# Performance work log

Hardware: AMD Instinct MI355X
Metric: run time of the kernel (lower is better)

## Reference

```python
import jax, jax.numpy as jnp
import numpy as np

# Module config (matches init_kwargs)
SHAPE = (32, 32)          # wire grid
KERNEL = (3, 3)           # window per dim
NUM_LAYERS = 4
NINPUTS = int(np.prod(KERNEL))        # 9
NPOS = 2 ** NINPUTS                   # 512 possible boolean input combos


def _bitmask():
    # itertools.product(range(2), repeat=NINPUTS) then transpose -> (NINPUTS, NPOS)
    # combination j, window-element m has bit (j >> (NINPUTS-1-m)) & 1
    j = jnp.arange(NPOS)
    m = jnp.arange(NINPUTS)
    return ((j[None, :] >> (NINPUTS - 1 - m)[:, None]) & 1).astype(jnp.float32)


def _convolve(x):
    # x: (B, H, W) -> (B, H, W, K) wrapped sliding windows (im2col via rolls),
    # faithful to ASIC.convolve with kernel_offset='center'.
    out = x
    for d, k in enumerate(KERNEL):
        # window element i along dim d comes from position +i (wraparound)
        out = jnp.stack([jnp.roll(out, -i, axis=1 + d) for i in range(k)], axis=out.ndim)
    out = out.reshape(x.shape + (-1,))  # (B, H, W, K) with k0 slowest-varying
    # 'center' offset: roll by prod((k-1)//2) along the LAST spatial dim (as the torch code does)
    shift = int(np.prod([(k - 1) // 2 for k in KERNEL]))
    out = jnp.roll(out, shift, axis=len(KERNEL))  # axis = last spatial axis in (B, H, W, K)
    return out


def setup_inputs() -> dict:
    key = jax.random.key(0)
    k1, k2 = jax.random.split(key)
    x = jax.random.uniform(k1, (16,) + SHAPE, dtype=jnp.float32)
    toggle_gates = jax.random.uniform(k2, (NUM_LAYERS, NPOS) + SHAPE, dtype=jnp.float32)
    return {"x": x, "toggle_gates": toggle_gates}


def reference(x, toggle_gates):
    tw = jax.nn.sigmoid(toggle_gates)       # (L, NPOS, H, W)
    bits = _bitmask()                        # (NINPUTS, NPOS)
    # embed(): shape == x spatial shape -> stride-1 slices; initial state is x, output is full state
    state = x                                # (B, H, W)
    for layer in range(NUM_LAYERS):
        conv = _convolve(state)              # (B, H, W, K)
        # soft-LUT weights: prod over window elems of (1 - |bit - input|)
        w = jnp.prod(1.0 - jnp.abs(conv[..., None] - bits), axis=-2)  # (B, H, W, NPOS)
        state = jnp.clip(jnp.einsum('bhwp,phw->bhw', w, tw[layer]), 0.0, 1.0)
    return state
```

## Files before the change

kernel.cpp:

```cpp
#include <hip/hip_runtime.h>

#define HH 32
#define WW 32
#define NPOS 512
#define TILE 8
#define PPAD 516
#define NTHR 512
#define NBLK 128
#define NLAYERS 4
#define RPAD 33
#define FSTR 16
#define FLAGV(L) (0x5EED0001 + (L))

__device__ __forceinline__ float ld_dev(const float* p) {
    return __hip_atomic_load(p, __ATOMIC_RELAXED, __HIP_MEMORY_SCOPE_AGENT);
}
__device__ __forceinline__ void st_dev(float* p, float v) {
    __hip_atomic_store(p, v, __ATOMIC_RELAXED, __HIP_MEMORY_SCOPE_AGENT);
}

__device__ __forceinline__ void neighbor_sync(int* flags, int layer, int h, int seg) {
    __syncthreads();
    const int t = threadIdx.x;
    if (t == 0) {
        __hip_atomic_store(&flags[(layer * NBLK + (h * 4 + seg)) * FSTR], FLAGV(layer),
                           __ATOMIC_RELAXED, __HIP_MEMORY_SCOPE_AGENT);
    }
    if (t < 9) {
        int dr = t / 3, ds = t % 3 - 1;
        int pid = (((h + dr) & 31) << 2) | ((seg + ds) & 3);
        const int* f = &flags[(layer * NBLK + pid) * FSTR];
        while (__hip_atomic_load(f, __ATOMIC_RELAXED, __HIP_MEMORY_SCOPE_AGENT) != FLAGV(layer)) {
            __builtin_amdgcn_s_sleep(2);
        }
    }
    __syncthreads();
}

__device__ __forceinline__ void make_v(const float c[9], float* v) {
    float a2[2], a4[4], a8[8], a16[16];
    a2[0] = 1.0f - c[4]; a2[1] = c[4];
    #pragma unroll
    for (int i = 0; i < 2; ++i)  { a4[2*i]  = a2[i]  * (1.0f - c[5]); a4[2*i+1]  = a2[i]  * c[5]; }
    #pragma unroll
    for (int i = 0; i < 4; ++i)  { a8[2*i]  = a4[i]  * (1.0f - c[6]); a8[2*i+1]  = a4[i]  * c[6]; }
    #pragma unroll
    for (int i = 0; i < 8; ++i)  { a16[2*i] = a8[i]  * (1.0f - c[7]); a16[2*i+1] = a8[i]  * c[7]; }
    #pragma unroll
    for (int i = 0; i < 16; ++i) { v[2*i]   = a16[i] * (1.0f - c[8]); v[2*i+1]   = a16[i] * c[8]; }
}

__device__ __forceinline__ float sigm(float g) {
    return __builtin_amdgcn_rcpf(1.0f + __expf(-g));
}

__global__ __launch_bounds__(NTHR) void asic_fused(
    const float* __restrict__ x,
    const float* __restrict__ tg,
    float* __restrict__ bufA,
    float* __restrict__ bufB,
    float* __restrict__ bufC,
    float* __restrict__ out,
    int* __restrict__ flags)
{
    __shared__ float  lut[NLAYERS][TILE * PPAD];
    __shared__ float2 red[2][8 * RPAD];

    const int t   = threadIdx.x;
    const int bid = blockIdx.x;
    const int h   = bid & 31;
    const int seg = bid >> 5;
    const int w0  = seg * TILE;
    const int hw0 = h * 32 + w0;

    const int th    = t & 255;
    const int bhalf = t >> 8;
    const int hwl   = th & 7;
    const int bp    = (th >> 3) & 3;
    const int oct   = th >> 5;
    const int w     = w0 + hwl;
    const int b0    = bhalf * 8 + 2 * bp;
    const int bit0 = (oct >> 2) & 1, bit1 = (oct >> 1) & 1, bit2 = oct & 1;

    #pragma unroll
    for (int k = 0; k < 2; ++k) {
        int f    = t + NTHR * k;
        int p    = f >> 1;
        int half = f & 1;
        float4 g4 = *(const float4*)(tg + p * (HH * WW) + hw0 + half * 4);
        int pb = half * 4;
        lut[0][(pb + 0) * PPAD + p] = sigm(g4.x);
        lut[0][(pb + 1) * PPAD + p] = sigm(g4.y);
        lut[0][(pb + 2) * PPAD + p] = sigm(g4.z);
        lut[0][(pb + 3) * PPAD + p] = sigm(g4.w);
    }

    float c0[9], c1[9];
    {
        const float* s0 = x + b0 * (HH * WW);
        const float* s1 = s0 + (HH * WW);
        #pragma unroll
        for (int i = 0; i < 3; ++i) {
            int row = ((h + i) & 31) * 32;
            #pragma unroll
            for (int j = 0; j < 3; ++j) {
                int idx = row + ((w + j - 1 + 32) & 31);
                c0[3 * i + j] = s0[idx];
                c1[3 * i + j] = s1[idx];
            }
        }
    }

    __syncthreads();

    #pragma unroll
    for (int k = 0; k < 6; ++k) {
        int f     = t + NTHR * k;
        int layer = 1 + (f >> 10);
        int r     = f & 1023;
        int p     = r >> 1;
        int half  = r & 1;
        float4 g4 = *(const float4*)(tg + (size_t)layer * NPOS * HH * WW + p * (HH * WW) + hw0 + half * 4);
        int pb = half * 4;
        lut[layer][(pb + 0) * PPAD + p] = sigm(g4.x);
        lut[layer][(pb + 1) * PPAD + p] = sigm(g4.y);
        lut[layer][(pb + 2) * PPAD + p] = sigm(g4.z);
        lut[layer][(pb + 3) * PPAD + p] = sigm(g4.w);
    }

    float* dsts[NLAYERS] = {bufA, bufB, bufC, out};
    const float* src = x;

    for (int layer = 0; layer < NLAYERS; ++layer) {
        float* dst = dsts[layer];

        if (layer > 0) {
            const float* s0 = src + b0 * (HH * WW);
            const float* s1 = s0 + (HH * WW);
            #pragma unroll
            for (int i = 0; i < 3; ++i) {
                int row = ((h + i) & 31) * 32;
                #pragma unroll
                for (int j = 0; j < 3; ++j) {
                    int idx = row + ((w + j - 1 + 32) & 31);
                    c0[3 * i + j] = ld_dev(s0 + idx);
                    c1[3 * i + j] = ld_dev(s1 + idx);
                }
            }
        }

        float v0[32], v1[32];
        make_v(c0, v0);
        make_v(c1, v1);

        float base0 = (bit0 ? c0[0] : 1.0f - c0[0]) * (bit1 ? c0[1] : 1.0f - c0[1]) * (bit2 ? c0[2] : 1.0f - c0[2]);
        float base1 = (bit0 ? c1[0] : 1.0f - c1[0]) * (bit1 ? c1[1] : 1.0f - c1[1]) * (bit2 ? c1[2] : 1.0f - c1[2]);
        float uA0 = base0 * (1.0f - c0[3]), uB0 = base0 * c0[3];
        float uA1 = base1 * (1.0f - c1[3]), uB1 = base1 * c1[3];

        const float4* lutp = (const float4*)(&lut[layer][0] + hwl * PPAD);
        const float4* A = lutp + (2 * oct) * 8;
        const float4* B = A + 8;
        float sA0 = 0.f, sA1 = 0.f, sB0 = 0.f, sB1 = 0.f;
        #pragma unroll
        for (int l4 = 0; l4 < 8; ++l4) {
            float4 LA = A[l4];
            float4 LB = B[l4];
            sA0 = fmaf(LA.x, v0[4*l4+0], sA0); sA0 = fmaf(LA.y, v0[4*l4+1], sA0);
            sA0 = fmaf(LA.z, v0[4*l4+2], sA0); sA0 = fmaf(LA.w, v0[4*l4+3], sA0);
            sA1 = fmaf(LA.x, v1[4*l4+0], sA1); sA1 = fmaf(LA.y, v1[4*l4+1], sA1);
            sA1 = fmaf(LA.z, v1[4*l4+2], sA1); sA1 = fmaf(LA.w, v1[4*l4+3], sA1);
            sB0 = fmaf(LB.x, v0[4*l4+0], sB0); sB0 = fmaf(LB.y, v0[4*l4+1], sB0);
            sB0 = fmaf(LB.z, v0[4*l4+2], sB0); sB0 = fmaf(LB.w, v0[4*l4+3], sB0);
            sB1 = fmaf(LB.x, v1[4*l4+0], sB1); sB1 = fmaf(LB.y, v1[4*l4+1], sB1);
            sB1 = fmaf(LB.z, v1[4*l4+2], sB1); sB1 = fmaf(LB.w, v1[4*l4+3], sB1);
        }
        float acc0 = fmaf(uA0, sA0, uB0 * sB0);
        float acc1 = fmaf(uA1, sA1, uB1 * sB1);

        red[bhalf][oct * RPAD + bp * 8 + hwl] = make_float2(acc0, acc1);
        __syncthreads();

        if (th < 64) {
            int hw  = th & 7;
            int bl  = th >> 3;
            int bpi = bl >> 1, par = bl & 1;
            float s = 0.0f;
            #pragma unroll
            for (int o = 0; o < 8; ++o) {
                float2 r = red[bhalf][o * RPAD + bpi * 8 + hw];
                s += par ? r.y : r.x;
            }
            s = fminf(fmaxf(s, 0.0f), 1.0f);
            st_dev(dst + (size_t)(bhalf * 8 + bl) * (HH * WW) + h * 32 + w0 + hw, s);
        }

        if (layer < NLAYERS - 1) neighbor_sync(flags, layer, h, seg);
        src = dst;
    }
}

extern "C" void kernel_launch(void* const* d_in, const int* in_sizes, int n_in,
                              void* d_out, int out_size, void* d_ws, size_t ws_size,
                              hipStream_t stream) {
    const float* x  = (const float*)d_in[0];
    const float* tg = (const float*)d_in[1];
    float* out  = (float*)d_out;
    float* bufA = (float*)d_ws;
    float* bufB = bufA + 16 * HH * WW;
    float* bufC = bufB + 16 * HH * WW;
    int*   flags = (int*)((char*)d_ws + 256 * 1024);

    asic_fused<<<NBLK, NTHR, 0, stream>>>(x, tg, bufA, bufB, bufC, out, flags);
}
```

Before: 71.41 us.

## Halve spatial tile width and double block count to spread work across more CUs

Changes the tile from 8 to 4 columns per block and launches 256 blocks instead of 128, so each block handles all 16 batches for 4 positions. The thread mapping is remapped so each thread covers 32 LUT entries (16 octets via 4 fixed leading bits) instead of 64, and the reduction is widened to 16 partial sums. LUT loading per block halves. The neighbor flag indexing is updated for 8 segments per row. This trades more blocks and more flags to poll against less per-block serial work and lower latency per layer.

Result: slower. 75.77 us (+6.1%).

```diff
diff --git a/kernel.cpp b/kernel.cpp
--- a/kernel.cpp
+++ b/kernel.cpp
@@ -3,12 +3,11 @@
 #define HH 32
 #define WW 32
 #define NPOS 512
-#define TILE 8
+#define TILE 4
 #define PPAD 516
 #define NTHR 512
-#define NBLK 128
+#define NBLK 256
 #define NLAYERS 4
-#define RPAD 33
 #define FSTR 16
 #define FLAGV(L) (0x5EED0001 + (L))
 
@@ -23,12 +22,12 @@
     __syncthreads();
     const int t = threadIdx.x;
     if (t == 0) {
-        __hip_atomic_store(&flags[(layer * NBLK + (h * 4 + seg)) * FSTR], FLAGV(layer),
+        __hip_atomic_store(&flags[(layer * NBLK + (h * 8 + seg)) * FSTR], FLAGV(layer),
                            __ATOMIC_RELAXED, __HIP_MEMORY_SCOPE_AGENT);
     }
     if (t < 9) {
         int dr = t / 3, ds = t % 3 - 1;
-        int pid = (((h + dr) & 31) << 2) | ((seg + ds) & 3);
+        int pid = (((h + dr) & 31) * 8) | ((seg + ds) & 7);
         const int* f = &flags[(layer * NBLK + pid) * FSTR];
         while (__hip_atomic_load(f, __ATOMIC_RELAXED, __HIP_MEMORY_SCOPE_AGENT) != FLAGV(layer)) {
             __builtin_amdgcn_s_sleep(2);
@@ -64,7 +63,7 @@
     int* __restrict__ flags)
 {
     __shared__ float  lut[NLAYERS][TILE * PPAD];
-    __shared__ float2 red[2][8 * RPAD];
+    __shared__ float2 red[16][33];
 
     const int t   = threadIdx.x;
     const int bid = blockIdx.x;
@@ -73,26 +72,20 @@
     const int w0  = seg * TILE;
     const int hw0 = h * 32 + w0;
 
-    const int th    = t & 255;
-    const int bhalf = t >> 8;
-    const int hwl   = th & 7;
-    const int bp    = (th >> 3) & 3;
-    const int oct   = th >> 5;
-    const int w     = w0 + hwl;
-    const int b0    = bhalf * 8 + 2 * bp;
-    const int bit0 = (oct >> 2) & 1, bit1 = (oct >> 1) & 1, bit2 = oct & 1;
+    const int hwl = t & 3;
+    const int bp  = (t >> 2) & 7;
+    const int oct = t >> 5;
+    const int w   = w0 + hwl;
+    const int b0  = 2 * bp;
+    const int bit0 = (oct >> 3) & 1, bit1 = (oct >> 2) & 1;
+    const int bit2 = (oct >> 1) & 1, bit3 = oct & 1;
 
-    #pragma unroll
-    for (int k = 0; k < 2; ++k) {
-        int f    = t + NTHR * k;
-        int p    = f >> 1;
-        int half = f & 1;
-        float4 g4 = *(const float4*)(tg + p * (HH * WW) + hw0 + half * 4);
-        int pb = half * 4;
-        lut[0][(pb + 0) * PPAD + p] = sigm(g4.x);
-        lut[0][(pb + 1) * PPAD + p] = sigm(g4.y);
-        lut[0][(pb + 2) * PPAD + p] = sigm(g4.z);
-        lut[0][(pb + 3) * PPAD + p] = sigm(g4.w);
+    {
+        float4 g4 = *(const float4*)(tg + t * (HH * WW) + hw0);
+        lut[0][0 * PPAD + t] = sigm(g4.x);
+        lut[0][1 * PPAD + t] = sigm(g4.y);
+        lut[0][2 * PPAD + t] = sigm(g4.z);
+        lut[0][3 * PPAD + t] = sigm(g4.w);
     }
 
     float c0[9], c1[9];
@@ -114,18 +107,12 @@
     __syncthreads();
 
     #pragma unroll
-    for (int k = 0; k < 6; ++k) {
-        int f     = t + NTHR * k;
-        int layer = 1 + (f >> 10);
-        int r     = f & 1023;
-        int p     = r >> 1;
-        int half  = r & 1;
-        float4 g4 = *(const float4*)(tg + (size_t)layer * NPOS * HH * WW + p * (HH * WW) + hw0 + half * 4);
-        int pb = half * 4;
-        lut[layer][(pb + 0) * PPAD + p] = sigm(g4.x);
-        lut[layer][(pb + 1) * PPAD + p] = sigm(g4.y);
-        lut[layer][(pb + 2) * PPAD + p] = sigm(g4.z);
-        lut[layer][(pb + 3) * PPAD + p] = sigm(g4.w);
+    for (int layer = 1; layer < NLAYERS; ++layer) {
+        float4 g4 = *(const float4*)(tg + (size_t)layer * NPOS * HH * WW + t * (HH * WW) + hw0);
+        lut[layer][0 * PPAD + t] = sigm(g4.x);
+        lut[layer][1 * PPAD + t] = sigm(g4.y);
+        lut[layer][2 * PPAD + t] = sigm(g4.z);
+        lut[layer][3 * PPAD + t] = sigm(g4.w);
     }
 
     float* dsts[NLAYERS] = {bufA, bufB, bufC, out};
@@ -153,46 +140,37 @@
         make_v(c0, v0);
         make_v(c1, v1);
 
-        float base0 = (bit0 ? c0[0] : 1.0f - c0[0]) * (bit1 ? c0[1] : 1.0f - c0[1]) * (bit2 ? c0[2] : 1.0f - c0[2]);
-        float base1 = (bit0 ? c1[0] : 1.0f - c1[0]) * (bit1 ? c1[1] : 1.0f - c1[1]) * (bit2 ? c1[2] : 1.0f - c1[2]);
-        float uA0 = base0 * (1.0f - c0[3]), uB0 = base0 * c0[3];
-        float uA1 = base1 * (1.0f - c1[3]), uB1 = base1 * c1[3];
+        float u0 = (bit0 ? c0[0] : 1.0f - c0[0]) * (bit1 ? c0[1] : 1.0f - c0[1])
+                 * (bit2 ? c0[2] : 1.0f - c0[2]) * (bit3 ? c0[3] : 1.0f - c0[3]);
+        float u1 = (bit0 ? c1[0] : 1.0f - c1[0]) * (bit1 ? c1[1] : 1.0f - c1[1])
+                 * (bit2 ? c1[2] : 1.0f - c1[2]) * (bit3 ? c1[3] : 1.0f - c1[3]);
 
-        const float4* lutp = (const float4*)(&lut[layer][0] + hwl * PPAD);
-        const float4* A = lutp + (2 * oct) * 8;
-        const float4* B = A + 8;
-        float sA0 = 0.f, sA1 = 0.f, sB0 = 0.f, sB1 = 0.f;
+        const float4* A = (const float4*)(&lut[layer][0] + hwl * PPAD) + oct * 8;
+        float sA0 = 0.f, sA1 = 0.f;
         #pragma unroll
         for (int l4 = 0; l4 < 8; ++l4) {
             float4 LA = A[l4];
-            float4 LB = B[l4];
             sA0 = fmaf(LA.x, v0[4*l4+0], sA0); sA0 = fmaf(LA.y, v0[4*l4+1], sA0);
             sA0 = fmaf(LA.z, v0[4*l4+2], sA0); sA0 = fmaf(LA.w, v0[4*l4+3], sA0);
             sA1 = fmaf(LA.x, v1[4*l4+0], sA1); sA1 = fmaf(LA.y, v1[4*l4+1], sA1);
             sA1 = fmaf(LA.z, v1[4*l4+2], sA1); sA1 = fmaf(LA.w, v1[4*l4+3], sA1);
-            sB0 = fmaf(LB.x, v0[4*l4+0], sB0); sB0 = fmaf(LB.y, v0[4*l4+1], sB0);
-            sB0 = fmaf(LB.z, v0[4*l4+2], sB0); sB0 = fmaf(LB.w, v0[4*l4+3], sB0);
-            sB1 = fmaf(LB.x, v1[4*l4+0], sB1); sB1 = fmaf(LB.y, v1[4*l4+1], sB1);
-            sB1 = fmaf(LB.z, v1[4*l4+2], sB1); sB1 = fmaf(LB.w, v1[4*l4+3], sB1);
         }
-        float acc0 = fmaf(uA0, sA0, uB0 * sB0);
-        float acc1 = fmaf(uA1, sA1, uB1 * sB1);
 
-        red[bhalf][oct * RPAD + bp * 8 + hwl] = make_float2(acc0, acc1);
+        red[oct][t & 31] = make_float2(u0 * sA0, u1 * sA1);
         __syncthreads();
 
-        if (th < 64) {
-            int hw  = th & 7;
-            int bl  = th >> 3;
-            int bpi = bl >> 1, par = bl & 1;
+        if (t < 64) {
+            int pos = t & 3;
+            int bpi = (t >> 2) & 7;
+            int par = t >> 5;
             float s = 0.0f;
             #pragma unroll
-            for (int o = 0; o < 8; ++o) {
-                float2 r = red[bhalf][o * RPAD + bpi * 8 + hw];
+            for (int g = 0; g < 16; ++g) {
+                float2 r = red[g][bpi * 4 + pos];
                 s += par ? r.y : r.x;
             }
             s = fminf(fmaxf(s, 0.0f), 1.0f);
-            st_dev(dst + (size_t)(bhalf * 8 + bl) * (HH * WW) + h * 32 + w0 + hw, s);
+            st_dev(dst + (size_t)(2 * bpi + par) * (HH * WW) + h * 32 + w0 + pos, s);
         }
 
         if (layer < NLAYERS - 1) neighbor_sync(flags, layer, h, seg);
```
